# Performance work log

Hardware: AMD Instinct MI355X
Metric: run time of the kernel (lower is better)

Reference implementation:

```python
import jax, jax.numpy as jnp
import numpy as np

B = 1024
N_SPEC = 2048
R1 = 20000
R2 = 40000


def setup_inputs() -> dict:
    key = jax.random.key(0)
    k1, k2, k3, k4, k5, k6, k7 = jax.random.split(key, 7)
    return {
        "y_in": jax.random.uniform(k1, (B, N_SPEC), dtype=jnp.float32),
        "rates_1st": jax.random.uniform(k2, (B, R1), dtype=jnp.float32),
        "rates_2nd": jax.random.uniform(k3, (B, R2), dtype=jnp.float32),
        "inds_1r": jax.random.randint(k4, (R1,), 0, N_SPEC, dtype=jnp.int32),
        "inds_1p": jax.random.randint(k5, (R1,), 0, N_SPEC, dtype=jnp.int32),
        "inds_2r": jax.random.randint(k6, (R2, 2), 0, N_SPEC, dtype=jnp.int32),
        "inds_2p": jax.random.randint(k7, (R2,), 0, N_SPEC, dtype=jnp.int32),
    }


def reference(y_in, rates_1st, rates_2nd, inds_1r, inds_1p, inds_2r, inds_2p):
    # First-order reactions: gather reactant abundance, scale by rate,
    # scatter-add into product species.  y_in: [B, S]
    term_1 = y_in[:, inds_1r] * rates_1st                      # [B, R1]
    # Second-order reactions: product of the two reactant abundances.
    term_2 = y_in[:, inds_2r[:, 0]] * y_in[:, inds_2r[:, 1]] * rates_2nd  # [B, R2]
    y_out = jnp.zeros_like(y_in)
    y_out = y_out.at[:, inds_1p].add(term_1)
    y_out = y_out.at[:, inds_2p].add(term_2)
    return y_out
```

## Files before the change

### kernel.cpp

```cpp
#include <hip/hip_runtime.h>


#define NSPEC 2048
#define BDIM  1024
#define R1    20000
#define R2    40000
#define CH    5000
#define NCH1  (R1 / CH)
#define NCH2  (R2 / CH)
#define NCH   (NCH1 + NCH2)

#define WS_PTRR 0
#define WS_E1P  (NCH * NSPEC * 4)
#define WS_CSR2 (WS_E1P + R1 * 4)

__global__ __launch_bounds__(1024) void k_build(
    const int* __restrict__ inds_1r,
    const int* __restrict__ inds_1p, const int* __restrict__ inds_2p,
    uint* __restrict__ ptrr, uint* __restrict__ e1p, ushort* __restrict__ csr2)
{
    __shared__ uint cnt[NSPEC];
    __shared__ uint part[1024];
    __shared__ uint h2[64];
    __shared__ uint off[64];

    const int c   = blockIdx.x;
    const int tid = threadIdx.x;

    cnt[tid] = 0u; cnt[tid + 1024] = 0u;
    __syncthreads();

    const bool first = (c < NCH1);
    const int  base  = first ? c * CH : (c - NCH1) * CH;
    const int* __restrict__ prod = first ? (inds_1p + base) : (inds_2p + base);

    for (int i = tid; i < CH; i += 1024)
        atomicAdd(&cnt[prod[i]], 1u);
    __syncthreads();

    uint v0 = cnt[2 * tid], v1 = cnt[2 * tid + 1];
    uint tsum = v0 + v1;
    part[tid] = tsum;
    __syncthreads();
    for (int o = 1; o < 1024; o <<= 1) {
        uint x = (tid >= o) ? part[tid - o] : 0u;
        __syncthreads();
        part[tid] += x;
        __syncthreads();
    }
    const uint run  = part[tid] - tsum;
    const uint beg0 = run, beg1 = run + v0;
    cnt[2 * tid]     = beg0;
    cnt[2 * tid + 1] = beg1;
    if (tid < 64) h2[tid] = 0u;
    __syncthreads();

    if (first) {
        for (int i = tid; i < CH; i += 1024) {
            const int s = prod[i];
            const uint pos = atomicAdd(&cnt[s], 1u);
            e1p[c * CH + i] = (uint)inds_1r[base + i] | (pos << 11);
        }
    } else {
        for (int i = tid; i < CH; i += 1024) {
            const int s = prod[i];
            const uint pos = atomicAdd(&cnt[s], 1u);
            csr2[base + i] = (ushort)pos;
        }
    }
    const uint b0 = min(v0, 63u), b1 = min(v1, 63u);
    atomicAdd(&h2[b0], 1u);
    atomicAdd(&h2[b1], 1u);
    __syncthreads();

    if (tid == 0) {
        uint a = 0;
        for (int v = 63; v >= 0; --v) { off[v] = a; a += h2[v]; }
    }
    __syncthreads();

    const uint r0 = atomicAdd(&off[b0], 1u);
    const uint r1 = atomicAdd(&off[b1], 1u);
    ptrr[c * NSPEC + r0] = beg0 | (min(v0, 255u) << 13) | ((uint)(2 * tid) << 21);
    ptrr[c * NSPEC + r1] = beg1 | (min(v1, 255u) << 13) | ((uint)(2 * tid + 1) << 21);
}

#define MBLOCK 512

__global__ __launch_bounds__(MBLOCK, 8) void k_main(
    const float* __restrict__ y_in,
    const float* __restrict__ rates_1st,
    const float* __restrict__ rates_2nd,
    const int*   __restrict__ inds_2r,
    const uint*  __restrict__ ptrr,
    const uint*  __restrict__ e1p,
    const ushort* __restrict__ csr2,
    float*       __restrict__ y_out)
{
    __shared__ float ys[NSPEC];
    __shared__ float accl[NSPEC];
    __shared__ float tl[CH];

    const int b   = blockIdx.x;
    const int tid = threadIdx.x;

    ((float4*)ys)[tid] = ((const float4*)(y_in + (size_t)b * NSPEC))[tid];
    ((float4*)accl)[tid] = make_float4(0.f, 0.f, 0.f, 0.f);
    __syncthreads();

    for (int c = 0; c < NCH; ++c) {
        if (c < NCH1) {
            const uint4*  ev = (const uint4*) (e1p + c * CH);
            const float4* rv = (const float4*)(rates_1st + (size_t)b * R1 + c * CH);
            for (int i = tid; i < CH / 4; i += MBLOCK) {
                const uint4  e = ev[i];
                const float4 q = rv[i];
                tl[e.x >> 11] = ys[e.x & 2047u] * q.x;
                tl[e.y >> 11] = ys[e.y & 2047u] * q.y;
                tl[e.z >> 11] = ys[e.z & 2047u] * q.z;
                tl[e.w >> 11] = ys[e.w & 2047u] * q.w;
            }
        } else {
            const int c2 = c - NCH1;
            const uint4*   iv = (const uint4*)  (inds_2r + 2 * (c2 * CH));
            const float4*  rv = (const float4*) (rates_2nd + (size_t)b * R2 + c2 * CH);
            const ushort4* pv = (const ushort4*)(csr2 + c2 * CH);
            for (int i = tid; i < CH / 4; i += MBLOCK) {
                const uint4   ia = iv[2 * i];
                const uint4   ib = iv[2 * i + 1];
                const float4  q  = rv[i];
                const ushort4 p  = pv[i];
                tl[p.x] = ys[ia.x] * ys[ia.y] * q.x;
                tl[p.y] = ys[ia.z] * ys[ia.w] * q.y;
                tl[p.z] = ys[ib.x] * ys[ib.y] * q.z;
                tl[p.w] = ys[ib.z] * ys[ib.w] * q.w;
            }
        }
        __syncthreads();

        const uint* pr = ptrr + c * NSPEC;
        #pragma unroll
        for (int k = 0; k < 4; ++k) {
            const uint v   = pr[k * MBLOCK + tid];
            uint       j   = v & 0x1FFFu;
            uint       n   = (v >> 13) & 0xFFu;
            const uint s   = v >> 21;
            float a = 0.f;
            for (; n > 0; --n, ++j) a += tl[j];
            accl[s] += a;
        }
        __syncthreads();
    }

    ((float4*)(y_out + (size_t)b * NSPEC))[tid] = ((const float4*)accl)[tid];
}

extern "C" void kernel_launch(void* const* d_in, const int* in_sizes, int n_in,
                              void* d_out, int out_size, void* d_ws, size_t ws_size,
                              hipStream_t stream) {
    const float* y_in      = (const float*)d_in[0];
    const float* rates_1st = (const float*)d_in[1];
    const float* rates_2nd = (const float*)d_in[2];
    const int*   inds_1r   = (const int*)d_in[3];
    const int*   inds_1p   = (const int*)d_in[4];
    const int*   inds_2r   = (const int*)d_in[5];
    const int*   inds_2p   = (const int*)d_in[6];
    float*       y_out     = (float*)d_out;

    char* ws = (char*)d_ws;
    uint*   ptrr = (uint*)  (ws + WS_PTRR);
    uint*   e1p  = (uint*)  (ws + WS_E1P);
    ushort* csr2 = (ushort*)(ws + WS_CSR2);

    k_build<<<NCH, 1024, 0, stream>>>(inds_1r, inds_1p, inds_2p, ptrr, e1p, csr2);
    k_main<<<BDIM, MBLOCK, 0, stream>>>(y_in, rates_1st, rates_2nd, inds_2r,
                                        ptrr, e1p, csr2, y_out);
}
```

Baseline: 331.8 us.

## Process two batch rows per block with interleaved float2 LDS and padded segments

Each block now handles two batch rows, storing y, accumulators and term buffers as interleaved float2, so index loads, the CSR pointer walk and the LDS gathers are shared across both rows. The chunk size is halved to fit the doubled LDS footprint, and the build kernel pads even-length product segments to odd widths, placed in length-sorted order, to spread float2 LDS bank accesses. This amortizes index traffic and per-segment loop overhead, at the cost of half as many blocks, lower occupancy (launch bound 4) and twice as many chunk barriers.

```diff
diff --git a/kernel.cpp b/kernel.cpp
--- a/kernel.cpp
+++ b/kernel.cpp
@@ -5,10 +5,11 @@
 #define BDIM  1024
 #define R1    20000
 #define R2    40000
-#define CH    5000
+#define CH    2500
 #define NCH1  (R1 / CH)
 #define NCH2  (R2 / CH)
 #define NCH   (NCH1 + NCH2)
+#define TLSZ  3780
 
 #define WS_PTRR 0
 #define WS_E1P  (NCH * NSPEC * 4)
@@ -21,6 +22,7 @@
 {
     __shared__ uint cnt[NSPEC];
     __shared__ uint part[1024];
+    __shared__ uint wbeg[NSPEC];
     __shared__ uint h2[64];
     __shared__ uint off[64];
 
@@ -38,9 +40,31 @@
         atomicAdd(&cnt[prod[i]], 1u);
     __syncthreads();
 
-    uint v0 = cnt[2 * tid], v1 = cnt[2 * tid + 1];
-    uint tsum = v0 + v1;
-    part[tid] = tsum;
+    const uint v0 = cnt[2 * tid], v1 = cnt[2 * tid + 1];
+
+    if (tid < 64) h2[tid] = 0u;
+    __syncthreads();
+    const uint b0 = min(v0, 63u), b1 = min(v1, 63u);
+    atomicAdd(&h2[b0], 1u);
+    atomicAdd(&h2[b1], 1u);
+    __syncthreads();
+    if (tid == 0) {
+        uint a = 0;
+        for (int v = 63; v >= 0; --v) { off[v] = a; a += h2[v]; }
+    }
+    __syncthreads();
+    const uint r0 = atomicAdd(&off[b0], 1u);
+    const uint r1 = atomicAdd(&off[b1], 1u);
+
+    const uint w0 = v0 + (((v0 & 1u) == 0u && v0 != 0u) ? 1u : 0u);
+    const uint w1 = v1 + (((v1 & 1u) == 0u && v1 != 0u) ? 1u : 0u);
+    wbeg[r0] = w0;
+    wbeg[r1] = w1;
+    __syncthreads();
+
+    const uint a0 = wbeg[2 * tid], a1 = wbeg[2 * tid + 1];
+    const uint ts = a0 + a1;
+    part[tid] = ts;
     __syncthreads();
     for (int o = 1; o < 1024; o <<= 1) {
         uint x = (tid >= o) ? part[tid - o] : 0u;
@@ -48,11 +72,16 @@
         part[tid] += x;
         __syncthreads();
     }
-    const uint run  = part[tid] - tsum;
-    const uint beg0 = run, beg1 = run + v0;
+    const uint run = part[tid] - ts;
+    wbeg[2 * tid]     = run;
+    wbeg[2 * tid + 1] = run + a0;
+    __syncthreads();
+
+    const uint beg0 = wbeg[r0], beg1 = wbeg[r1];
+    ptrr[c * NSPEC + r0] = beg0 | (min(v0, 255u) << 13) | ((uint)(2 * tid) << 21);
+    ptrr[c * NSPEC + r1] = beg1 | (min(v1, 255u) << 13) | ((uint)(2 * tid + 1) << 21);
     cnt[2 * tid]     = beg0;
     cnt[2 * tid + 1] = beg1;
-    if (tid < 64) h2[tid] = 0u;
     __syncthreads();
 
     if (first) {
@@ -68,26 +97,12 @@
             csr2[base + i] = (ushort)pos;
         }
     }
-    const uint b0 = min(v0, 63u), b1 = min(v1, 63u);
-    atomicAdd(&h2[b0], 1u);
-    atomicAdd(&h2[b1], 1u);
-    __syncthreads();
-
-    if (tid == 0) {
-        uint a = 0;
-        for (int v = 63; v >= 0; --v) { off[v] = a; a += h2[v]; }
-    }
-    __syncthreads();
-
-    const uint r0 = atomicAdd(&off[b0], 1u);
-    const uint r1 = atomicAdd(&off[b1], 1u);
-    ptrr[c * NSPEC + r0] = beg0 | (min(v0, 255u) << 13) | ((uint)(2 * tid) << 21);
-    ptrr[c * NSPEC + r1] = beg1 | (min(v1, 255u) << 13) | ((uint)(2 * tid + 1) << 21);
 }
 
 #define MBLOCK 512
-
-__global__ __launch_bounds__(MBLOCK, 8) void k_main(
+#define SPT    (NSPEC / MBLOCK)
+
+__global__ __launch_bounds__(MBLOCK, 4) void k_main(
     const float* __restrict__ y_in,
     const float* __restrict__ rates_1st,
     const float* __restrict__ rates_2nd,
@@ -97,62 +112,94 @@
     const ushort* __restrict__ csr2,
     float*       __restrict__ y_out)
 {
-    __shared__ float ys[NSPEC];
-    __shared__ float accl[NSPEC];
-    __shared__ float tl[CH];
-
-    const int b   = blockIdx.x;
+    __shared__ float2 ysi[NSPEC];
+    __shared__ float2 acci[NSPEC];
+    __shared__ float2 tli[TLSZ];
+
+    const int b2  = blockIdx.x * 2;
     const int tid = threadIdx.x;
 
-    ((float4*)ys)[tid] = ((const float4*)(y_in + (size_t)b * NSPEC))[tid];
-    ((float4*)accl)[tid] = make_float4(0.f, 0.f, 0.f, 0.f);
+    {
+        const float4 a = ((const float4*)(y_in + (size_t)b2 * NSPEC))[tid];
+        const float4 b = ((const float4*)(y_in + (size_t)(b2 + 1) * NSPEC))[tid];
+        ysi[4 * tid + 0] = make_float2(a.x, b.x);
+        ysi[4 * tid + 1] = make_float2(a.y, b.y);
+        ysi[4 * tid + 2] = make_float2(a.z, b.z);
+        ysi[4 * tid + 3] = make_float2(a.w, b.w);
+        acci[4 * tid + 0] = make_float2(0.f, 0.f);
+        acci[4 * tid + 1] = make_float2(0.f, 0.f);
+        acci[4 * tid + 2] = make_float2(0.f, 0.f);
+        acci[4 * tid + 3] = make_float2(0.f, 0.f);
+    }
     __syncthreads();
 
     for (int c = 0; c < NCH; ++c) {
         if (c < NCH1) {
-            const uint4*  ev = (const uint4*) (e1p + c * CH);
-            const float4* rv = (const float4*)(rates_1st + (size_t)b * R1 + c * CH);
+            const uint4*  ev  = (const uint4*) (e1p + c * CH);
+            const float4* q0v = (const float4*)(rates_1st + (size_t)b2 * R1 + c * CH);
+            const float4* q1v = (const float4*)(rates_1st + (size_t)(b2 + 1) * R1 + c * CH);
             for (int i = tid; i < CH / 4; i += MBLOCK) {
-                const uint4  e = ev[i];
-                const float4 q = rv[i];
-                tl[e.x >> 11] = ys[e.x & 2047u] * q.x;
-                tl[e.y >> 11] = ys[e.y & 2047u] * q.y;
-                tl[e.z >> 11] = ys[e.z & 2047u] * q.z;
-                tl[e.w >> 11] = ys[e.w & 2047u] * q.w;
+                const uint4  e  = ev[i];
+                const float4 q0 = q0v[i];
+                const float4 q1 = q1v[i];
+                float2 y;
+                y = ysi[e.x & 2047u]; tli[e.x >> 11] = make_float2(y.x * q0.x, y.y * q1.x);
+                y = ysi[e.y & 2047u]; tli[e.y >> 11] = make_float2(y.x * q0.y, y.y * q1.y);
+                y = ysi[e.z & 2047u]; tli[e.z >> 11] = make_float2(y.x * q0.z, y.y * q1.z);
+                y = ysi[e.w & 2047u]; tli[e.w >> 11] = make_float2(y.x * q0.w, y.y * q1.w);
             }
         } else {
             const int c2 = c - NCH1;
-            const uint4*   iv = (const uint4*)  (inds_2r + 2 * (c2 * CH));
-            const float4*  rv = (const float4*) (rates_2nd + (size_t)b * R2 + c2 * CH);
-            const ushort4* pv = (const ushort4*)(csr2 + c2 * CH);
+            const uint4*   iv  = (const uint4*)  (inds_2r + 2 * (c2 * CH));
+            const float4*  q0v = (const float4*) (rates_2nd + (size_t)b2 * R2 + c2 * CH);
+            const float4*  q1v = (const float4*) (rates_2nd + (size_t)(b2 + 1) * R2 + c2 * CH);
+            const ushort4* pv  = (const ushort4*)(csr2 + c2 * CH);
             for (int i = tid; i < CH / 4; i += MBLOCK) {
                 const uint4   ia = iv[2 * i];
                 const uint4   ib = iv[2 * i + 1];
-                const float4  q  = rv[i];
+                const float4  q0 = q0v[i];
+                const float4  q1 = q1v[i];
                 const ushort4 p  = pv[i];
-                tl[p.x] = ys[ia.x] * ys[ia.y] * q.x;
-                tl[p.y] = ys[ia.z] * ys[ia.w] * q.y;
-                tl[p.z] = ys[ib.x] * ys[ib.y] * q.z;
-                tl[p.w] = ys[ib.z] * ys[ib.w] * q.w;
+                float2 ya, yb;
+                ya = ysi[ia.x]; yb = ysi[ia.y];
+                tli[p.x] = make_float2(ya.x * yb.x * q0.x, ya.y * yb.y * q1.x);
+                ya = ysi[ia.z]; yb = ysi[ia.w];
+                tli[p.y] = make_float2(ya.x * yb.x * q0.y, ya.y * yb.y * q1.y);
+                ya = ysi[ib.x]; yb = ysi[ib.y];
+                tli[p.z] = make_float2(ya.x * yb.x * q0.z, ya.y * yb.y * q1.z);
+                ya = ysi[ib.z]; yb = ysi[ib.w];
+                tli[p.w] = make_float2(ya.x * yb.x * q0.w, ya.y * yb.y * q1.w);
             }
         }
         __syncthreads();
 
         const uint* pr = ptrr + c * NSPEC;
         #pragma unroll
-        for (int k = 0; k < 4; ++k) {
-            const uint v   = pr[k * MBLOCK + tid];
-            uint       j   = v & 0x1FFFu;
-            uint       n   = (v >> 13) & 0xFFu;
-            const uint s   = v >> 21;
-            float a = 0.f;
-            for (; n > 0; --n, ++j) a += tl[j];
-            accl[s] += a;
-        }
-        __syncthreads();
-    }
-
-    ((float4*)(y_out + (size_t)b * NSPEC))[tid] = ((const float4*)accl)[tid];
+        for (int k = 0; k < SPT; ++k) {
+            const uint v = pr[k * MBLOCK + tid];
+            uint       j = v & 0x1FFFu;
+            uint       n = (v >> 13) & 0xFFu;
+            const uint s = v >> 21;
+            float a0 = 0.f, a1 = 0.f;
+            for (; n > 0; --n, ++j) {
+                const float2 t = tli[j];
+                a0 += t.x; a1 += t.y;
+            }
+            const float2 cu = acci[s];
+            acci[s] = make_float2(cu.x + a0, cu.y + a1);
+        }
+        __syncthreads();
+    }
+
+    float* o0 = y_out + (size_t)b2 * NSPEC;
+    float* o1 = o0 + NSPEC;
+    #pragma unroll
+    for (int k = 0; k < SPT; ++k) {
+        const int s = k * MBLOCK + tid;
+        const float2 v = acci[s];
+        o0[s] = v.x;
+        o1[s] = v.y;
+    }
 }
 
 extern "C" void kernel_launch(void* const* d_in, const int* in_sizes, int n_in,
@@ -173,6 +220,6 @@
     ushort* csr2 = (ushort*)(ws + WS_CSR2);
 
     k_build<<<NCH, 1024, 0, stream>>>(inds_1r, inds_1p, inds_2p, ptrr, e1p, csr2);
-    k_main<<<BDIM, MBLOCK, 0, stream>>>(y_in, rates_1st, rates_2nd, inds_2r,
-                                        ptrr, e1p, csr2, y_out);
+    k_main<<<BDIM / 2, MBLOCK, 0, stream>>>(y_in, rates_1st, rates_2nd, inds_2r,
+                                            ptrr, e1p, csr2, y_out);
 }
```

Result: no change. 333.9 us (+0.6%).
